# Kernel optimization log

Measured on AMD Instinct MI355X. Metric: run time of the kernel, lower is better.

The kernel has to match this reference:

```python
import jax, jax.numpy as jnp
import numpy as np

NUM_EXPERTS = 8
DIM = 1024
HIDDEN = 2048
N_TOKENS = 8192  # rows of x, includes padding beyond sum(num_tokens_per_expert)


def setup_inputs() -> dict:
    key = jax.random.key(0)
    k_x, k_w1, k_w2, k_w3 = jax.random.split(key, 4)
    x = jax.random.normal(k_x, (N_TOKENS, DIM), dtype=jnp.float32)
    # trunc_normal(std=0.02)-like init; w2 is zeros in torch init but we use
    w1 = jax.random.normal(k_w1, (NUM_EXPERTS, HIDDEN, DIM), dtype=jnp.float32) * 0.02
    w2 = jax.random.normal(k_w2, (NUM_EXPERTS, DIM, HIDDEN), dtype=jnp.float32) * 0.02
    w3 = jax.random.normal(k_w3, (NUM_EXPERTS, HIDDEN, DIM), dtype=jnp.float32) * 0.02
    # routed token counts per expert; sum <= N_TOKENS, remainder is padding
    num_tokens_per_expert = jnp.array([995, 1000, 980, 1010, 970, 1020, 990, 1005], dtype=jnp.int64)
    return {"x": x, "num_tokens_per_expert": num_tokens_per_expert,
            "w1": w1, "w2": w2, "w3": w3}


def reference(x, num_tokens_per_expert, w1, w2, w3):
    # Mirrors torch _run_experts_for_loop with act='silu'. The torch code calls
    # .tolist() on the counts (shapes are data-dependent), so we likewise treat
    # the per-expert counts as static host values.
    counts = np.asarray(num_tokens_per_expert).astype(np.int64)
    offsets = np.concatenate([np.zeros(1, np.int64), np.cumsum(counts)])
    total = int(offsets[-1])
    num_experts = w1.shape[0]
    out_splits = []
    for e in range(num_experts):
        xe = x[int(offsets[e]):int(offsets[e + 1])]            # [n_e, dim]
        gate = jax.nn.silu(xe @ w1[e].T)                       # [n_e, hidden]
        h = gate * (xe @ w3[e].T)                              # SwiGLU
        out_splits.append(h @ w2[e].T)                         # [n_e, dim]
    out = jnp.concatenate(out_splits, axis=0)
    num_padding = x.shape[0] - total
    if num_padding > 0:
        out = jnp.concatenate([out, jnp.zeros((num_padding, out.shape[-1]), out.dtype)], axis=0)
    return out
```

## Files before the change

### kernel.cpp

```cpp
#include <hip/hip_runtime.h>

#define NEXP 8
#define DIM  1024
#define HID  2048
#define NTOK 8192

#define BM 128
#define BN 128
#define BK 32
#define LDK 40

typedef short s16x8 __attribute__((ext_vector_type(8)));
typedef float f32x4 __attribute__((ext_vector_type(4)));
typedef unsigned short u16;

__device__ __forceinline__ u16 f2bf(float f) {
  unsigned int u = __builtin_bit_cast(unsigned int, f);
  u += 0x7FFFu + ((u >> 16) & 1u);
  return (u16)(u >> 16);
}

__device__ __forceinline__ void gload16(const u16* g, u16* l) {
  __builtin_amdgcn_global_load_lds((const __attribute__((address_space(1))) void*)g,
                                   (__attribute__((address_space(3))) void*)l, 16, 0, 0);
}

__device__ __forceinline__ bool find_tile(const int* __restrict__ cnts, int rt,
                                          int& e_out, int& row0, int& cnt_out, long long& off_out) {
  long long off = 0; int cum = 0;
  #pragma unroll
  for (int e = 0; e < NEXP; ++e) {
    int c = cnts[e];
    int nt = (c + BM - 1) / BM;
    if (rt < cum + nt) { e_out = e; row0 = (rt - cum) * BM; cnt_out = c; off_out = off; return true; }
    cum += nt; off += c;
  }
  return false;
}

__device__ __forceinline__ ushort4 cvt4(float4 a) {
  ushort4 r; r.x = f2bf(a.x); r.y = f2bf(a.y); r.z = f2bf(a.z); r.w = f2bf(a.w); return r;
}

__device__ __forceinline__ void cvt_region(const float* __restrict__ s, u16* __restrict__ d,
                                           int n4, int g, int T) {
  const float4* __restrict__ src = (const float4*)s;
  ushort4* __restrict__ dst = (ushort4*)d;
  int i = g;
  for (; i + 3 * T < n4; i += 4 * T) {
    const float4 a0 = src[i];
    const float4 a1 = src[i + T];
    const float4 a2 = src[i + 2 * T];
    const float4 a3 = src[i + 3 * T];
    dst[i]         = cvt4(a0);
    dst[i + T]     = cvt4(a1);
    dst[i + 2 * T] = cvt4(a2);
    dst[i + 3 * T] = cvt4(a3);
  }
  for (; i < n4; i += T) dst[i] = cvt4(src[i]);
}

__global__ __launch_bounds__(256) void cvt_multi(
    const float* __restrict__ s0, u16* __restrict__ d0, int n0,
    const float* __restrict__ s1, u16* __restrict__ d1, int n1,
    const float* __restrict__ s2, u16* __restrict__ d2, int n2,
    const float* __restrict__ s3, u16* __restrict__ d3, int n3) {
  const int T = gridDim.x * blockDim.x;
  const int g = blockIdx.x * blockDim.x + threadIdx.x;
  if (n0) cvt_region(s0, d0, n0, g, T);
  if (n1) cvt_region(s1, d1, n1, g, T);
  if (n2) cvt_region(s2, d2, n2, g, T);
  if (n3) cvt_region(s3, d3, n3, g, T);
}

#define XSTR 68
__global__ __launch_bounds__(512, 4) void gemm1_bf16(
    const u16* __restrict__ xb, const int* __restrict__ cnts,
    const u16* __restrict__ w1b, const u16* __restrict__ w3b,
    u16* __restrict__ hbuf)
{
  int e, row0, cnt; long long off;
  if (!find_tile(cnts, blockIdx.y, e, row0, cnt, off)) return;
  const int ct = blockIdx.x;

  __shared__ __align__(16) u16 smem[3 * 3 * 4096];
  u16* stage = smem;
  float* smem_f = (float*)smem;

  const int t    = threadIdx.x;
  const int lane = t & 63;
  const int wid  = t >> 6;
  const int mat  = wid >> 2;
  const int sw   = wid & 3;
  const int wr = sw >> 1, wc = sw & 1;
  const int lr = lane & 15;
  const int lk = (lane >> 4) * 8;

  const u16* xrow = xb + (size_t)(off + row0) * DIM;
  const u16* w1t  = w1b + ((size_t)e * HID + (size_t)ct * BN) * DIM;
  const u16* w3t  = w3b + ((size_t)e * HID + (size_t)ct * BN) * DIM;

  f32x4 acc[4][4];
  const f32x4 zf = {0.f, 0.f, 0.f, 0.f};
  #pragma unroll
  for (int i = 0; i < 4; ++i)
    #pragma unroll
    for (int j = 0; j < 4; ++j) acc[i][j] = zf;

  const int sidx = wid * 512 + lane * 8;
  const int srow = sidx >> 5;
  const int scol = sidx & 31;

  auto STAGE = [&](int k0, int b) {
    u16* base = stage + b * (3 * 4096);
    const size_t go = (size_t)srow * DIM + k0 + scol;
    gload16(&xrow[go], base        + wid * 512);
    gload16(&w1t [go], base + 4096 + wid * 512);
    gload16(&w3t [go], base + 8192 + wid * 512);
  };
  auto COMPUTE = [&](int b) {
    const u16* Asb = stage + b * (3 * 4096);
    const u16* Bsb = Asb + 4096 + mat * 4096;
    s16x8 af[4], bf[4];
    #pragma unroll
    for (int fm = 0; fm < 4; ++fm)
      af[fm] = *(const s16x8*)&Asb[(wr * 64 + fm * 16 + lr) * BK + lk];
    #pragma unroll
    for (int fn = 0; fn < 4; ++fn)
      bf[fn] = *(const s16x8*)&Bsb[(wc * 64 + fn * 16 + lr) * BK + lk];
    __builtin_amdgcn_s_setprio(1);
    #pragma unroll
    for (int fm = 0; fm < 4; ++fm)
      #pragma unroll
      for (int fn = 0; fn < 4; ++fn)
        acc[fm][fn] = __builtin_amdgcn_mfma_f32_16x16x32_bf16(af[fm], bf[fn], acc[fm][fn], 0, 0, 0);
    __builtin_amdgcn_s_setprio(0);
  };

  const int NT = DIM / BK;
  STAGE(0, 0);
  STAGE(BK, 1);
  for (int kt = 0; kt < NT; ++kt) {
    if (kt == NT - 1) { asm volatile("s_waitcnt vmcnt(0)" ::: "memory"); }
    else              { asm volatile("s_waitcnt vmcnt(3)" ::: "memory"); }
    __builtin_amdgcn_s_barrier();
    asm volatile("" ::: "memory");
    if (kt + 2 < NT) STAGE((kt + 2) * BK, (kt + 2) % 3);
    COMPUTE(kt % 3);
  }

  __syncthreads();
  if (mat) {
    float* up = smem_f + sw * (64 * XSTR);
    #pragma unroll
    for (int fm = 0; fm < 4; ++fm)
      #pragma unroll
      for (int fn = 0; fn < 4; ++fn)
        #pragma unroll
        for (int j = 0; j < 4; ++j)
          up[(fm * 16 + ((lane >> 4) << 2) + j) * XSTR + fn * 16 + lr] = acc[fm][fn][j];
  }
  __syncthreads();
  if (!mat) {
    const float* up = smem_f + sw * (64 * XSTR);
    #pragma unroll
    for (int fm = 0; fm < 4; ++fm)
      #pragma unroll
      for (int fn = 0; fn < 4; ++fn) {
        const int col = ct * BN + wc * 64 + fn * 16 + lr;
        #pragma unroll
        for (int j = 0; j < 4; ++j) {
          const int r = wr * 64 + fm * 16 + ((lane >> 4) << 2) + j;
          if (row0 + r < cnt) {
            const float gv = acc[fm][fn][j];
            const float uv = up[(fm * 16 + ((lane >> 4) << 2) + j) * XSTR + fn * 16 + lr];
            const float hv = (gv / (1.f + __expf(-gv))) * uv;
            hbuf[(size_t)(off + row0 + r) * HID + col] = f2bf(hv);
          }
        }
      }
  }
}

__global__ __launch_bounds__(256, 4) void gemm2_bf16(
    const u16* __restrict__ hbuf, const int* __restrict__ cnts,
    const u16* __restrict__ w2b, float* __restrict__ out)
{
  int e, row0, cnt; long long off;
  if (!find_tile(cnts, blockIdx.y, e, row0, cnt, off)) return;
  const int ct = blockIdx.x;

  __shared__ __align__(16) u16 stage[3 * 2 * 4096];

  const int t    = threadIdx.x;
  const int lane = t & 63;
  const int wid  = t >> 6;
  const int wr = wid >> 1, wc = wid & 1;
  const int lr = lane & 15;
  const int lk = (lane >> 4) * 8;

  const u16* arow = hbuf + (size_t)(off + row0) * HID;
  const u16* w2t  = w2b + ((size_t)e * DIM + (size_t)ct * BN) * HID;

  f32x4 acc[4][4];
  const f32x4 zf = {0.f, 0.f, 0.f, 0.f};
  #pragma unroll
  for (int i = 0; i < 4; ++i)
    #pragma unroll
    for (int j = 0; j < 4; ++j) acc[i][j] = zf;

  auto STAGE = [&](int k0, int b) {
    u16* base = stage + b * (2 * 4096);
    #pragma unroll
    for (int c = 0; c < 2; ++c) {
      const int chunk = wid * 2 + c;
      const int idx   = chunk * 512 + lane * 8;
      const int r  = idx >> 5;
      const int cc = idx & 31;
      const size_t go = (size_t)r * HID + k0 + cc;
      gload16(&arow[go], base        + chunk * 512);
      gload16(&w2t [go], base + 4096 + chunk * 512);
    }
  };
  auto COMPUTE = [&](int b) {
    const u16* Asb = stage + b * (2 * 4096);
    const u16* Bsb = Asb + 4096;
    s16x8 af[4], bf[4];
    #pragma unroll
    for (int fm = 0; fm < 4; ++fm)
      af[fm] = *(const s16x8*)&Asb[(wr * 64 + fm * 16 + lr) * BK + lk];
    #pragma unroll
    for (int fn = 0; fn < 4; ++fn)
      bf[fn] = *(const s16x8*)&Bsb[(wc * 64 + fn * 16 + lr) * BK + lk];
    #pragma unroll
    for (int fm = 0; fm < 4; ++fm)
      #pragma unroll
      for (int fn = 0; fn < 4; ++fn)
        acc[fm][fn] = __builtin_amdgcn_mfma_f32_16x16x32_bf16(af[fm], bf[fn], acc[fm][fn], 0, 0, 0);
  };

  const int NT = HID / BK;
  STAGE(0, 0);
  STAGE(BK, 1);
  for (int kt = 0; kt < NT; ++kt) {
    if (kt == NT - 1) { asm volatile("s_waitcnt vmcnt(0)" ::: "memory"); }
    else              { asm volatile("s_waitcnt vmcnt(4)" ::: "memory"); }
    __builtin_amdgcn_s_barrier();
    asm volatile("" ::: "memory");
    if (kt + 2 < NT) STAGE((kt + 2) * BK, (kt + 2) % 3);
    COMPUTE(kt % 3);
  }

  #pragma unroll
  for (int fm = 0; fm < 4; ++fm)
    #pragma unroll
    for (int fn = 0; fn < 4; ++fn) {
      const int col = ct * BN + wc * 64 + fn * 16 + lr;
      #pragma unroll
      for (int j = 0; j < 4; ++j) {
        const int r = wr * 64 + fm * 16 + ((lane >> 4) << 2) + j;
        if (row0 + r < cnt)
          out[(size_t)(off + row0 + r) * DIM + col] = acc[fm][fn][j];
      }
    }
}

__global__ __launch_bounds__(256) void gemm1_kernel(
    const float* __restrict__ x, const int* __restrict__ cnts,
    const float* __restrict__ w1, const float* __restrict__ w3,
    u16* __restrict__ hbuf)
{
  int e, row0, cnt; long long off;
  if (!find_tile(cnts, blockIdx.y, e, row0, cnt, off)) return;
  const int ct = blockIdx.x;

  __shared__ u16 As [BM * LDK];
  __shared__ u16 B1s[BN * LDK];
  __shared__ u16 B3s[BN * LDK];

  const int t    = threadIdx.x;
  const int srow = t >> 3;
  const int skq  = (t & 7) * 4;
  const int lane = t & 63;
  const int wid  = t >> 6;
  const int wr = wid >> 1, wc = wid & 1;
  const int lr = lane & 15;
  const int lk = (lane >> 4) * 8;

  const float* w1e = w1 + (size_t)e * HID * DIM;
  const float* w3e = w3 + (size_t)e * HID * DIM;

  f32x4 accg[4][4], accu[4][4];
  const f32x4 zf = {0.f, 0.f, 0.f, 0.f};
  #pragma unroll
  for (int i = 0; i < 4; ++i)
    #pragma unroll
    for (int j = 0; j < 4; ++j) { accg[i][j] = zf; accu[i][j] = zf; }

  for (int k0 = 0; k0 < DIM; k0 += BK) {
    __syncthreads();
    #pragma unroll
    for (int s = 0; s < 4; ++s) {
      const int r = s * 32 + srow;
      float4 va = make_float4(0.f, 0.f, 0.f, 0.f);
      const int gm = row0 + r;
      if (gm < cnt) va = *(const float4*)&x[(size_t)(off + gm) * DIM + k0 + skq];
      ushort4 ua; ua.x = f2bf(va.x); ua.y = f2bf(va.y); ua.z = f2bf(va.z); ua.w = f2bf(va.w);
      *(ushort4*)&As[r * LDK + skq] = ua;
      const size_t gb = (size_t)(ct * BN + r) * DIM + k0 + skq;
      const float4 v1 = *(const float4*)&w1e[gb];
      const float4 v3 = *(const float4*)&w3e[gb];
      ushort4 u1; u1.x = f2bf(v1.x); u1.y = f2bf(v1.y); u1.z = f2bf(v1.z); u1.w = f2bf(v1.w);
      ushort4 u3; u3.x = f2bf(v3.x); u3.y = f2bf(v3.y); u3.z = f2bf(v3.z); u3.w = f2bf(v3.w);
      *(ushort4*)&B1s[r * LDK + skq] = u1;
      *(ushort4*)&B3s[r * LDK + skq] = u3;
    }
    __syncthreads();

    s16x8 af[4], b1f[4], b3f[4];
    #pragma unroll
    for (int fm = 0; fm < 4; ++fm)
      af[fm] = *(const s16x8*)&As[(wr * 64 + fm * 16 + lr) * LDK + lk];
    #pragma unroll
    for (int fn = 0; fn < 4; ++fn) {
      b1f[fn] = *(const s16x8*)&B1s[(wc * 64 + fn * 16 + lr) * LDK + lk];
      b3f[fn] = *(const s16x8*)&B3s[(wc * 64 + fn * 16 + lr) * LDK + lk];
    }
    #pragma unroll
    for (int fm = 0; fm < 4; ++fm)
      #pragma unroll
      for (int fn = 0; fn < 4; ++fn) {
        accg[fm][fn] = __builtin_amdgcn_mfma_f32_16x16x32_bf16(af[fm], b1f[fn], accg[fm][fn], 0, 0, 0);
        accu[fm][fn] = __builtin_amdgcn_mfma_f32_16x16x32_bf16(af[fm], b3f[fn], accu[fm][fn], 0, 0, 0);
      }
  }

  #pragma unroll
  for (int fm = 0; fm < 4; ++fm)
    #pragma unroll
    for (int fn = 0; fn < 4; ++fn) {
      const f32x4 g = accg[fm][fn], u = accu[fm][fn];
      const int col = ct * BN + wc * 64 + fn * 16 + lr;
      #pragma unroll
      for (int j = 0; j < 4; ++j) {
        const int r = wr * 64 + fm * 16 + ((lane >> 4) << 2) + j;
        if (row0 + r < cnt) {
          const float gv = g[j];
          const float hv = (gv / (1.f + __expf(-gv))) * u[j];
          hbuf[(size_t)(off + row0 + r) * HID + col] = f2bf(hv);
        }
      }
    }
}

__global__ __launch_bounds__(256) void gemm2_kernel(
    const u16* __restrict__ hbuf, const int* __restrict__ cnts,
    const float* __restrict__ w2, float* __restrict__ out)
{
  int e, row0, cnt; long long off;
  if (!find_tile(cnts, blockIdx.y, e, row0, cnt, off)) return;
  const int ct = blockIdx.x;

  __shared__ u16 As[BM * LDK];
  __shared__ u16 Bs[BN * LDK];

  const int t    = threadIdx.x;
  const int srow = t >> 3;
  const int skq  = (t & 7) * 4;
  const int lane = t & 63;
  const int wid  = t >> 6;
  const int wr = wid >> 1, wc = wid & 1;
  const int lr = lane & 15;
  const int lk = (lane >> 4) * 8;

  const float* w2e = w2 + (size_t)e * DIM * HID;

  f32x4 acc[4][4];
  const f32x4 zf = {0.f, 0.f, 0.f, 0.f};
  #pragma unroll
  for (int i = 0; i < 4; ++i)
    #pragma unroll
    for (int j = 0; j < 4; ++j) acc[i][j] = zf;

  for (int k0 = 0; k0 < HID; k0 += BK) {
    __syncthreads();
    #pragma unroll
    for (int s = 0; s < 4; ++s) {
      const int r = s * 32 + srow;
      ushort4 ua = make_ushort4(0, 0, 0, 0);
      const int gm = row0 + r;
      if (gm < cnt) ua = *(const ushort4*)&hbuf[(size_t)(off + gm) * HID + k0 + skq];
      *(ushort4*)&As[r * LDK + skq] = ua;
      const float4 v2 = *(const float4*)&w2e[(size_t)(ct * BN + r) * HID + k0 + skq];
      ushort4 u2; u2.x = f2bf(v2.x); u2.y = f2bf(v2.y); u2.z = f2bf(v2.z); u2.w = f2bf(v2.w);
      *(ushort4*)&Bs[r * LDK + skq] = u2;
    }
    __syncthreads();

    s16x8 af[4], bf[4];
    #pragma unroll
    for (int fm = 0; fm < 4; ++fm)
      af[fm] = *(const s16x8*)&As[(wr * 64 + fm * 16 + lr) * LDK + lk];
    #pragma unroll
    for (int fn = 0; fn < 4; ++fn)
      bf[fn] = *(const s16x8*)&Bs[(wc * 64 + fn * 16 + lr) * LDK + lk];
    #pragma unroll
    for (int fm = 0; fm < 4; ++fm)
      #pragma unroll
      for (int fn = 0; fn < 4; ++fn)
        acc[fm][fn] = __builtin_amdgcn_mfma_f32_16x16x32_bf16(af[fm], bf[fn], acc[fm][fn], 0, 0, 0);
  }

  #pragma unroll
  for (int fm = 0; fm < 4; ++fm)
    #pragma unroll
    for (int fn = 0; fn < 4; ++fn) {
      const int col = ct * BN + wc * 64 + fn * 16 + lr;
      #pragma unroll
      for (int j = 0; j < 4; ++j) {
        const int r = wr * 64 + fm * 16 + ((lane >> 4) << 2) + j;
        if (row0 + r < cnt)
          out[(size_t)(off + row0 + r) * DIM + col] = acc[fm][fn][j];
      }
    }
}

__global__ void zero_pad_kernel(const int* __restrict__ cnts, float* __restrict__ out)
{
  int total = 0;
  #pragma unroll
  for (int e = 0; e < NEXP; ++e) total += cnts[e];
  const int row = blockIdx.x;
  if (row < total) return;
  float4* p = (float4*)(out + (size_t)row * DIM);
  p[threadIdx.x] = make_float4(0.f, 0.f, 0.f, 0.f);
}

extern "C" void kernel_launch(void* const* d_in, const int* in_sizes, int n_in,
                              void* d_out, int out_size, void* d_ws, size_t ws_size,
                              hipStream_t stream) {
  const float* x    = (const float*)d_in[0];
  const int*   cnts = (const int*)d_in[1];
  const float* w1   = (const float*)d_in[2];
  const float* w2   = (const float*)d_in[3];
  const float* w3   = (const float*)d_in[4];
  float*       out  = (float*)d_out;

  const size_t HBUF_E = (size_t)NTOK * HID;
  const size_t XB_E   = (size_t)NTOK * DIM;
  const size_t W_E    = (size_t)NEXP * HID * DIM;
  const size_t need_min  = (HBUF_E + XB_E + 2 * W_E) * sizeof(u16);
  const size_t need_full = (HBUF_E + XB_E + 3 * W_E) * sizeof(u16);

  u16* hbuf = (u16*)d_ws;
  dim3 blk(256);
  const int XB4 = (int)(XB_E / 4), W4 = (int)(W_E / 4);

  if (ws_size >= need_full) {
    u16* xb = hbuf + HBUF_E;
    u16* wA = xb + XB_E;
    u16* wB = wA + W_E;
    u16* wC = wB + W_E;
    cvt_multi<<<dim3(2048), blk, 0, stream>>>(x, xb, XB4, w1, wA, W4, w3, wB, W4, w2, wC, W4);
    gemm1_bf16<<<dim3(HID / BN, 72), dim3(512), 0, stream>>>(xb, cnts, wA, wB, hbuf);
    gemm2_bf16<<<dim3(DIM / BN, 72), blk, 0, stream>>>(hbuf, cnts, wC, out);
  } else if (ws_size >= need_min) {
    u16* xb = hbuf + HBUF_E;
    u16* wA = xb + XB_E;
    u16* wB = wA + W_E;
    cvt_multi<<<dim3(2048), blk, 0, stream>>>(x, xb, XB4, w1, wA, W4, w3, wB, W4, (const float*)nullptr, (u16*)nullptr, 0);
    gemm1_bf16<<<dim3(HID / BN, 72), dim3(512), 0, stream>>>(xb, cnts, wA, wB, hbuf);
    cvt_multi<<<dim3(2048), blk, 0, stream>>>(w2, wA, W4, (const float*)nullptr, (u16*)nullptr, 0,
                                              (const float*)nullptr, (u16*)nullptr, 0,
                                              (const float*)nullptr, (u16*)nullptr, 0);
    gemm2_bf16<<<dim3(DIM / BN, 72), blk, 0, stream>>>(hbuf, cnts, wA, out);
  } else {
    gemm1_kernel<<<dim3(HID / BN, 72), blk, 0, stream>>>(x, cnts, w1, w3, hbuf);
    gemm2_kernel<<<dim3(DIM / BN, 72), blk, 0, stream>>>(hbuf, cnts, w2, out);
  }
  zero_pad_kernel<<<dim3(NTOK), dim3(256), 0, stream>>>(cnts, out);
}
```

Before: 208.4 us.

## Overlap w2 bf16 conversion with gemm1 and XOR-swizzle LDS tile layout

Moves the fp32-to-bf16 conversion of w2 out of the up-front conversion kernel and into extra blocks of the gemm1 launch, so that conversion runs alongside the first GEMM instead of before it. It also applies an XOR swizzle to the column chunk used by the global-to-LDS staging and the matching fragment reads in both GEMMs, aiming to reduce LDS bank conflicts. The added converter blocks compete with GEMM tiles for CUs and bandwidth. The swizzle must stay consistent between the write and read index maps to give correct results.

```diff
diff --git a/kernel.cpp b/kernel.cpp
--- a/kernel.cpp
+++ b/kernel.cpp
@@ -9,6 +9,7 @@
 #define BN 128
 #define BK 32
 #define LDK 40
+#define CVTY 16
 
 typedef short s16x8 __attribute__((ext_vector_type(8)));
 typedef float f32x4 __attribute__((ext_vector_type(4)));
@@ -18,6 +19,10 @@
   unsigned int u = __builtin_bit_cast(unsigned int, f);
   u += 0x7FFFu + ((u >> 16) & 1u);
   return (u16)(u >> 16);
+}
+
+__device__ __forceinline__ ushort4 cvt4(float4 a) {
+  ushort4 r; r.x = f2bf(a.x); r.y = f2bf(a.y); r.z = f2bf(a.z); r.w = f2bf(a.w); return r;
 }
 
 __device__ __forceinline__ void gload16(const u16* g, u16* l) {
@@ -36,10 +41,6 @@
     cum += nt; off += c;
   }
   return false;
-}
-
-__device__ __forceinline__ ushort4 cvt4(float4 a) {
-  ushort4 r; r.x = f2bf(a.x); r.y = f2bf(a.y); r.z = f2bf(a.z); r.w = f2bf(a.w); return r;
 }
 
 __device__ __forceinline__ void cvt_region(const float* __restrict__ s, u16* __restrict__ d,
@@ -77,10 +78,33 @@
 __global__ __launch_bounds__(512, 4) void gemm1_bf16(
     const u16* __restrict__ xb, const int* __restrict__ cnts,
     const u16* __restrict__ w1b, const u16* __restrict__ w3b,
-    u16* __restrict__ hbuf)
+    u16* __restrict__ hbuf,
+    const float* __restrict__ w2f, u16* __restrict__ wC, int nW4)
 {
+  if (blockIdx.y < CVTY) {
+    if (nW4) {
+      const int cb = blockIdx.y * gridDim.x + blockIdx.x;
+      const int T  = CVTY * gridDim.x * 512;
+      int i = cb * 512 + threadIdx.x;
+      const float4* __restrict__ src = (const float4*)w2f;
+      ushort4* __restrict__ dst = (ushort4*)wC;
+      for (; i + 3 * T < nW4; i += 4 * T) {
+        const float4 a0 = src[i];
+        const float4 a1 = src[i + T];
+        const float4 a2 = src[i + 2 * T];
+        const float4 a3 = src[i + 3 * T];
+        dst[i]         = cvt4(a0);
+        dst[i + T]     = cvt4(a1);
+        dst[i + 2 * T] = cvt4(a2);
+        dst[i + 3 * T] = cvt4(a3);
+      }
+      for (; i < nW4; i += T) dst[i] = cvt4(src[i]);
+    }
+    return;
+  }
+
   int e, row0, cnt; long long off;
-  if (!find_tile(cnts, blockIdx.y, e, row0, cnt, off)) return;
+  if (!find_tile(cnts, blockIdx.y - CVTY, e, row0, cnt, off)) return;
   const int ct = blockIdx.x;
 
   __shared__ __align__(16) u16 smem[3 * 3 * 4096];
@@ -94,7 +118,7 @@
   const int sw   = wid & 3;
   const int wr = sw >> 1, wc = sw & 1;
   const int lr = lane & 15;
-  const int lk = (lane >> 4) * 8;
+  const int lk = (((lane >> 4) ^ ((lr >> 1) & 3)) << 3);
 
   const u16* xrow = xb + (size_t)(off + row0) * DIM;
   const u16* w1t  = w1b + ((size_t)e * HID + (size_t)ct * BN) * DIM;
@@ -107,9 +131,10 @@
     #pragma unroll
     for (int j = 0; j < 4; ++j) acc[i][j] = zf;
 
-  const int sidx = wid * 512 + lane * 8;
-  const int srow = sidx >> 5;
-  const int scol = sidx & 31;
+  const int q    = lane >> 2;
+  const int cf   = (lane & 3) ^ ((q >> 1) & 3);
+  const int srow = wid * 16 + q;
+  const int scol = cf * 8;
 
   auto STAGE = [&](int k0, int b) {
     u16* base = stage + b * (3 * 4096);
@@ -197,7 +222,7 @@
   const int wid  = t >> 6;
   const int wr = wid >> 1, wc = wid & 1;
   const int lr = lane & 15;
-  const int lk = (lane >> 4) * 8;
+  const int lk = (((lane >> 4) ^ ((lr >> 1) & 3)) << 3);
 
   const u16* arow = hbuf + (size_t)(off + row0) * HID;
   const u16* w2t  = w2b + ((size_t)e * DIM + (size_t)ct * BN) * HID;
@@ -209,15 +234,16 @@
     #pragma unroll
     for (int j = 0; j < 4; ++j) acc[i][j] = zf;
 
+  const int q  = lane >> 2;
+  const int cf = (lane & 3) ^ ((q >> 1) & 3);
+
   auto STAGE = [&](int k0, int b) {
     u16* base = stage + b * (2 * 4096);
     #pragma unroll
     for (int c = 0; c < 2; ++c) {
       const int chunk = wid * 2 + c;
-      const int idx   = chunk * 512 + lane * 8;
-      const int r  = idx >> 5;
-      const int cc = idx & 31;
-      const size_t go = (size_t)r * HID + k0 + cc;
+      const int r = chunk * 16 + q;
+      const size_t go = (size_t)r * HID + k0 + cf * 8;
       gload16(&arow[go], base        + chunk * 512);
       gload16(&w2t [go], base + 4096 + chunk * 512);
     }
@@ -461,15 +487,18 @@
     u16* wA = xb + XB_E;
     u16* wB = wA + W_E;
     u16* wC = wB + W_E;
-    cvt_multi<<<dim3(2048), blk, 0, stream>>>(x, xb, XB4, w1, wA, W4, w3, wB, W4, w2, wC, W4);
-    gemm1_bf16<<<dim3(HID / BN, 72), dim3(512), 0, stream>>>(xb, cnts, wA, wB, hbuf);
+    cvt_multi<<<dim3(2048), blk, 0, stream>>>(x, xb, XB4, w1, wA, W4, w3, wB, W4,
+                                              (const float*)nullptr, (u16*)nullptr, 0);
+    gemm1_bf16<<<dim3(HID / BN, 72 + CVTY), dim3(512), 0, stream>>>(xb, cnts, wA, wB, hbuf, w2, wC, W4);
     gemm2_bf16<<<dim3(DIM / BN, 72), blk, 0, stream>>>(hbuf, cnts, wC, out);
   } else if (ws_size >= need_min) {
     u16* xb = hbuf + HBUF_E;
     u16* wA = xb + XB_E;
     u16* wB = wA + W_E;
-    cvt_multi<<<dim3(2048), blk, 0, stream>>>(x, xb, XB4, w1, wA, W4, w3, wB, W4, (const float*)nullptr, (u16*)nullptr, 0);
-    gemm1_bf16<<<dim3(HID / BN, 72), dim3(512), 0, stream>>>(xb, cnts, wA, wB, hbuf);
+    cvt_multi<<<dim3(2048), blk, 0, stream>>>(x, xb, XB4, w1, wA, W4, w3, wB, W4,
+                                              (const float*)nullptr, (u16*)nullptr, 0);
+    gemm1_bf16<<<dim3(HID / BN, 72 + CVTY), dim3(512), 0, stream>>>(xb, cnts, wA, wB, hbuf,
+                                                                    (const float*)nullptr, (u16*)nullptr, 0);
     cvt_multi<<<dim3(2048), blk, 0, stream>>>(w2, wA, W4, (const float*)nullptr, (u16*)nullptr, 0,
                                               (const float*)nullptr, (u16*)nullptr, 0,
                                               (const float*)nullptr, (u16*)nullptr, 0);
```

New measurement: 197.7 us. 1.05x faster.
